# Kernel optimization log

Hardware: AMD Instinct MI355X
Metric: run time of the kernel (lower is better)

Reference implementation:

```python
import jax, jax.numpy as jnp
import numpy as np

EMBED = 512
HEADS = 8
HEAD_DIM = EMBED // HEADS
N, T = 512, 64


def setup_inputs() -> dict:
    key = jax.random.key(0)
    ks = jax.random.split(key, 11)
    s = 1.0 / np.sqrt(EMBED)
    inp = {
        'values': jax.random.normal(ks[0], (N, T, EMBED), jnp.float32),
        'keys':   jax.random.normal(ks[1], (N, T, EMBED), jnp.float32),
        'query':  jax.random.normal(ks[2], (N, T, EMBED), jnp.float32),
        'Wv': jax.random.uniform(ks[3], (EMBED, EMBED), jnp.float32, -s, s),
        'bv': jax.random.uniform(ks[4], (EMBED,), jnp.float32, -s, s),
        'Wk': jax.random.uniform(ks[5], (EMBED, EMBED), jnp.float32, -s, s),
        'bk': jax.random.uniform(ks[6], (EMBED,), jnp.float32, -s, s),
        'Wq': jax.random.uniform(ks[7], (EMBED, EMBED), jnp.float32, -s, s),
        'bq': jax.random.uniform(ks[8], (EMBED,), jnp.float32, -s, s),
        'Wo': jax.random.uniform(ks[9], (EMBED, EMBED), jnp.float32, -s, s),
        'bo': jax.random.uniform(ks[10], (EMBED,), jnp.float32, -s, s),
    }
    return inp


def reference(values, keys, query, Wv, bv, Wk, bk, Wq, bq, Wo, bo):
    n, t, c = query.shape
    v = (values @ Wv.T + bv).reshape(n, t, HEADS, HEAD_DIM)
    k = (keys   @ Wk.T + bk).reshape(n, t, HEADS, HEAD_DIM)
    q = (query  @ Wq.T + bq).reshape(n, t, HEADS, HEAD_DIM)
    # attention over the batch axis: energy[q,k,t,h]
    energy = jnp.einsum('qthd,kthd->qkth', q, k)
    attn = jax.nn.softmax(energy / jnp.sqrt(jnp.float32(EMBED)), axis=1)
    out = jnp.einsum('qkth,kthd->qthd', attn, v).reshape(n, t, HEADS * HEAD_DIM)
    return out @ Wo.T + bo
```

## Files before the change

kernel.cpp:

```cpp
#include <hip/hip_runtime.h>
#include <hip/hip_bf16.h>
#include <math.h>

#define NBATCH 512
#define TT 64
#define EMB 512
#define NHEADS 8
#define HDIM 64
#define MROWS (NBATCH * TT)
#define ROWSTRIDE (TT * EMB)
#define WSEG 262144

static constexpr float QSCALE = 0.0637587140f;

typedef __attribute__((ext_vector_type(8))) short short8v;
typedef __attribute__((ext_vector_type(4))) float f32x4;

__device__ __forceinline__ unsigned short f2bf(float x) {
    union { float f; unsigned int u; } v; v.f = x;
    unsigned int r = v.u + 0x7fff + ((v.u >> 16) & 1);
    return (unsigned short)(r >> 16);
}

__device__ __forceinline__ unsigned int cvtpk(float lo, float hi) {
    unsigned int r;
    asm("v_cvt_pk_bf16_f32 %0, %1, %2" : "=v"(r) : "v"(lo), "v"(hi));
    return r;
}

__device__ __forceinline__ void gl16(const void* g, void* l) {
    __builtin_amdgcn_global_load_lds(
        (const __attribute__((address_space(1))) unsigned int*)g,
        (__attribute__((address_space(3))) unsigned int*)l, 16, 0, 0);
}

__global__ __launch_bounds__(256) void cvtw(
    const float* __restrict__ w0, const float* __restrict__ w1,
    const float* __restrict__ w2, const float* __restrict__ w3,
    unsigned short* __restrict__ dst)
{
    const int seg = blockIdx.y;
    const float* src = (seg == 0) ? w0 : (seg == 1) ? w1 : (seg == 2) ? w2 : w3;
    const float sc = (seg == 0) ? QSCALE : 1.0f;
    const size_t i = (size_t)blockIdx.x * 256 + threadIdx.x;
    float4 v = reinterpret_cast<const float4*>(src)[i];
    ushort4 r;
    r.x = f2bf(v.x * sc); r.y = f2bf(v.y * sc); r.z = f2bf(v.z * sc); r.w = f2bf(v.w * sc);
    reinterpret_cast<ushort4*>(dst + (size_t)seg * WSEG)[i] = r;
}

__global__ __launch_bounds__(256) void gemm_proj3(
    const float* __restrict__ A0, const float* __restrict__ A1,
    const float* __restrict__ A2, const unsigned short* __restrict__ Wb,
    const float* __restrict__ b0, const float* __restrict__ b1, const float* __restrict__ b2,
    unsigned short* __restrict__ o0, unsigned short* __restrict__ o1, unsigned short* __restrict__ o2)
{
    __shared__ __align__(16) float Asf[128 * 32];
    __shared__ __align__(16) unsigned short Bs[128 * 32];
    const int z = blockIdx.z;
    const float* A = (z == 0) ? A0 : (z == 1) ? A1 : A2;
    const unsigned short* W = Wb + (size_t)z * WSEG;
    const float* bias = (z == 0) ? b0 : (z == 1) ? b1 : b2;
    const float bsc = (z == 0) ? QSCALE : 1.0f;
    unsigned short* Cout = (z == 0) ? o0 : (z == 1) ? o1 : o2;

    const int tid = threadIdx.x;
    const int wave = tid >> 6, lane = tid & 63;
    const int lg = lane >> 4, li = lane & 15;
    const int m0 = blockIdx.x * 128;
    const int n0 = blockIdx.y * 128;
    const int wr = (wave >> 1) * 64;
    const int wc = (wave & 1) * 64;

    f32x4 acc[4][4] = {};

    const int asrc_unit = (tid & 7) ^ ((tid >> 3) & 7);
    const float* gaf = A + (size_t)(m0 + (tid >> 3)) * 512 + asrc_unit * 4;
    float* lA = Asf + wave * 256;
    const unsigned short* gb = W + (size_t)(n0 + (tid >> 2)) * 512 + (tid & 3) * 8;
    unsigned short* lB = &Bs[wave * 512];

    for (int k0 = 0; k0 < 512; k0 += 32) {
        __syncthreads();
        gl16(gaf + k0, lA);
        gl16(gaf + k0 + 32 * 512, lA + 1024);
        gl16(gaf + k0 + 64 * 512, lA + 2048);
        gl16(gaf + k0 + 96 * 512, lA + 3072);
        gl16(gb + k0, lB);
        gl16(gb + k0 + 64 * 512, lB + 2048);
        __syncthreads();

        short8v af[4], bfr[4];
#pragma unroll
        for (int i = 0; i < 4; i++) {
            const int r = wr + i * 16 + li;
            const int rx = r & 7;
            const float4 fa = *reinterpret_cast<const float4*>(
                &Asf[r * 32 + ((lg * 2) ^ rx) * 4]);
            const float4 fb = *reinterpret_cast<const float4*>(
                &Asf[r * 32 + ((lg * 2 + 1) ^ rx) * 4]);
            union { unsigned int u[4]; short8v v; } pk;
            pk.u[0] = cvtpk(fa.x, fa.y); pk.u[1] = cvtpk(fa.z, fa.w);
            pk.u[2] = cvtpk(fb.x, fb.y); pk.u[3] = cvtpk(fb.z, fb.w);
            af[i] = pk.v;
            bfr[i] = *reinterpret_cast<const short8v*>(&Bs[(wc + i * 16 + li) * 32 + lg * 8]);
        }
#pragma unroll
        for (int i = 0; i < 4; i++)
#pragma unroll
            for (int j = 0; j < 4; j++)
                acc[i][j] = __builtin_amdgcn_mfma_f32_16x16x32_bf16(af[i], bfr[j], acc[i][j], 0, 0, 0);
    }

#pragma unroll
    for (int j = 0; j < 4; j++) {
        const int col = n0 + wc + j * 16 + li;
        const float bb = bias[col] * bsc;
#pragma unroll
        for (int i = 0; i < 4; i++) {
            const int row0 = m0 + wr + i * 16 + lg * 4;
#pragma unroll
            for (int r = 0; r < 4; r++)
                Cout[(size_t)(row0 + r) * 512 + col] = f2bf(acc[i][j][r] + bb);
        }
    }
}

__global__ __launch_bounds__(256) void gemm_out(
    const unsigned short* __restrict__ A, const unsigned short* __restrict__ W,
    const float* __restrict__ bias, float* __restrict__ Cout)
{
    __shared__ __align__(16) unsigned short As[128 * 32];
    __shared__ __align__(16) unsigned short Bs[128 * 32];
    const int tid = threadIdx.x;
    const int wave = tid >> 6, lane = tid & 63;
    const int lg = lane >> 4, li = lane & 15;
    const int m0 = blockIdx.x * 128;
    const int n0 = blockIdx.y * 128;
    const int wr = (wave >> 1) * 64;
    const int wc = (wave & 1) * 64;

    f32x4 acc[4][4] = {};

    const unsigned short* ga = A + (size_t)(m0 + (tid >> 2)) * 512 + (tid & 3) * 8;
    const unsigned short* gb = W + (size_t)(n0 + (tid >> 2)) * 512 + (tid & 3) * 8;
    unsigned short* lA = &As[wave * 512];
    unsigned short* lB = &Bs[wave * 512];

    for (int k0 = 0; k0 < 512; k0 += 32) {
        __syncthreads();
        gl16(ga + k0, lA);
        gl16(ga + k0 + 64 * 512, lA + 2048);
        gl16(gb + k0, lB);
        gl16(gb + k0 + 64 * 512, lB + 2048);
        __syncthreads();

        short8v af[4], bfr[4];
#pragma unroll
        for (int i = 0; i < 4; i++) {
            af[i]  = *reinterpret_cast<const short8v*>(&As[(wr + i * 16 + li) * 32 + lg * 8]);
            bfr[i] = *reinterpret_cast<const short8v*>(&Bs[(wc + i * 16 + li) * 32 + lg * 8]);
        }
#pragma unroll
        for (int i = 0; i < 4; i++)
#pragma unroll
            for (int j = 0; j < 4; j++)
                acc[i][j] = __builtin_amdgcn_mfma_f32_16x16x32_bf16(af[i], bfr[j], acc[i][j], 0, 0, 0);
    }

#pragma unroll
    for (int j = 0; j < 4; j++) {
        const int col = n0 + wc + j * 16 + li;
        const float bb = bias[col];
#pragma unroll
        for (int i = 0; i < 4; i++) {
            const int row0 = m0 + wr + i * 16 + lg * 4;
#pragma unroll
            for (int r = 0; r < 4; r++)
                Cout[(size_t)(row0 + r) * 512 + col] = acc[i][j][r] + bb;
        }
    }
}

__global__ __launch_bounds__(256) void attn_bf16(
    const unsigned short* __restrict__ qp, const unsigned short* __restrict__ kp,
    const unsigned short* __restrict__ vp, unsigned short* __restrict__ ao)
{
    __shared__ __align__(16) unsigned short Qs[128 * 64];
    __shared__ __align__(16) unsigned short Ks[64 * 64];
    __shared__ __align__(16) unsigned short Vt[64][68];
    __shared__ __align__(16) unsigned short Pl[4][32][72];

    const int tid = threadIdx.x;
    const int wave = tid >> 6, lane = tid & 63;
    const int lg = lane >> 4, li = lane & 15;
    const int n0 = blockIdx.x * 128;
    const int th = blockIdx.y;
    const size_t base = (size_t)(th >> 3) * EMB + (size_t)(th & 7) * HDIM;

    {
        const unsigned short* gq = qp + (size_t)(n0 + (tid >> 3)) * ROWSTRIDE + base + (tid & 7) * 8;
        unsigned short* lq = &Qs[wave * 512];
#pragma unroll
        for (int i = 0; i < 4; i++)
            gl16(gq + (size_t)i * 32 * ROWSTRIDE, lq + i * 2048);
    }
    __syncthreads();
    short8v qf[2][2];
#pragma unroll
    for (int mf = 0; mf < 2; mf++)
#pragma unroll
        for (int kf = 0; kf < 2; kf++)
            qf[mf][kf] = *reinterpret_cast<const short8v*>(
                &Qs[(wave * 32 + mf * 16 + li) * 64 + kf * 32 + lg * 8]);

    const int vd0 = (tid & 15) * 4;
    const int vk0 = (tid >> 4) * 4;
    const unsigned short* gv = vp + base + vd0;
    uint2 vl[4];
#pragma unroll
    for (int i = 0; i < 4; i++)
        vl[i] = *reinterpret_cast<const uint2*>(gv + (size_t)(vk0 + i) * ROWSTRIDE);

    const short8v ones = (short8v)(short)0x3F80;
    f32x4 acc[2][4] = {};
    f32x4 acc_l[2] = {};

    for (int kv = 0; kv < 8; kv++) {
        const int k0 = kv * 64;
        __syncthreads();

        {
            unsigned short* lk = &Ks[wave * 512];
#pragma unroll
            for (int i = 0; i < 2; i++) {
                const int r = (tid >> 3) + i * 32;
                const int srcofs = (((tid & 7) * 8) ^ ((r & 7) * 8));
                gl16(kp + (size_t)(k0 + r) * ROWSTRIDE + base + srcofs, lk + i * 2048);
            }
        }
#pragma unroll
        for (int dd = 0; dd < 4; dd++) {
            const unsigned int sel = (dd & 1) ? 0x07060302u : 0x05040100u;
            const unsigned int a = (dd < 2) ? vl[0].x : vl[0].y;
            const unsigned int b = (dd < 2) ? vl[1].x : vl[1].y;
            const unsigned int c = (dd < 2) ? vl[2].x : vl[2].y;
            const unsigned int d = (dd < 2) ? vl[3].x : vl[3].y;
            uint2 o;
            o.x = __builtin_amdgcn_perm(b, a, sel);
            o.y = __builtin_amdgcn_perm(d, c, sel);
            *reinterpret_cast<uint2*>(&Vt[vd0 + dd][vk0]) = o;
        }
        __syncthreads();

        if (kv < 7) {
#pragma unroll
            for (int i = 0; i < 4; i++)
                vl[i] = *reinterpret_cast<const uint2*>(
                    gv + (size_t)(k0 + 64 + vk0 + i) * ROWSTRIDE);
        }

        f32x4 s[2][4] = {};
#pragma unroll
        for (int nf = 0; nf < 4; nf++) {
            const int key = nf * 16 + li;
#pragma unroll
            for (int kf = 0; kf < 2; kf++) {
                const short8v kfrag = *reinterpret_cast<const short8v*>(
                    &Ks[key * 64 + ((kf * 32 + lg * 8) ^ ((key & 7) * 8))]);
#pragma unroll
                for (int mf = 0; mf < 2; mf++)
                    s[mf][nf] = __builtin_amdgcn_mfma_f32_16x16x32_bf16(kfrag, qf[mf][kf], s[mf][nf], 0, 0, 0);
            }
        }

#pragma unroll
        for (int mf = 0; mf < 2; mf++)
#pragma unroll
            for (int nf = 0; nf < 4; nf++) {
                const float p0 = exp2f(s[mf][nf][0]);
                const float p1 = exp2f(s[mf][nf][1]);
                const float p2 = exp2f(s[mf][nf][2]);
                const float p3 = exp2f(s[mf][nf][3]);
                union { unsigned int u[2]; uint2 v; } pk2;
                pk2.u[0] = cvtpk(p0, p1);
                pk2.u[1] = cvtpk(p2, p3);
                *reinterpret_cast<uint2*>(&Pl[wave][mf * 16 + li][nf * 16 + lg * 4]) = pk2.v;
            }

        short8v pf[2][2];
#pragma unroll
        for (int mf = 0; mf < 2; mf++)
#pragma unroll
            for (int kf = 0; kf < 2; kf++)
                pf[mf][kf] = *reinterpret_cast<const short8v*>(
                    &Pl[wave][mf * 16 + li][kf * 32 + lg * 8]);
#pragma unroll
        for (int mf = 0; mf < 2; mf++)
#pragma unroll
            for (int kf = 0; kf < 2; kf++)
                acc_l[mf] = __builtin_amdgcn_mfma_f32_16x16x32_bf16(pf[mf][kf], ones, acc_l[mf], 0, 0, 0);

#pragma unroll
        for (int df = 0; df < 4; df++)
#pragma unroll
            for (int kf = 0; kf < 2; kf++) {
                const short8v vfr = *reinterpret_cast<const short8v*>(
                    &Vt[df * 16 + li][kf * 32 + lg * 8]);
#pragma unroll
                for (int mf = 0; mf < 2; mf++)
                    acc[mf][df] = __builtin_amdgcn_mfma_f32_16x16x32_bf16(pf[mf][kf], vfr, acc[mf][df], 0, 0, 0);
            }
    }

#pragma unroll
    for (int mf = 0; mf < 2; mf++) {
#pragma unroll
        for (int r = 0; r < 4; r++) {
            const float linv = 1.0f / acc_l[mf][r];
            const int qrow = n0 + wave * 32 + mf * 16 + lg * 4 + r;
#pragma unroll
            for (int df = 0; df < 4; df++)
                ao[(size_t)qrow * ROWSTRIDE + base + df * 16 + li] = f2bf(acc[mf][df][r] * linv);
        }
    }
}

extern "C" void kernel_launch(void* const* d_in, const int* in_sizes, int n_in,
                              void* d_out, int out_size, void* d_ws, size_t ws_size,
                              hipStream_t stream) {
    const float* values = (const float*)d_in[0];
    const float* keys   = (const float*)d_in[1];
    const float* query  = (const float*)d_in[2];
    const float* Wv = (const float*)d_in[3];
    const float* bv = (const float*)d_in[4];
    const float* Wk = (const float*)d_in[5];
    const float* bk = (const float*)d_in[6];
    const float* Wq = (const float*)d_in[7];
    const float* bq = (const float*)d_in[8];
    const float* Wo = (const float*)d_in[9];
    const float* bo = (const float*)d_in[10];
    float* out = (float*)d_out;

    unsigned short* ws16 = (unsigned short*)d_ws;
    const size_t PLANE = (size_t)MROWS * EMB;
    unsigned short* qb = ws16;
    unsigned short* kb = ws16 + PLANE;
    unsigned short* vb = ws16 + 2 * PLANE;
    unsigned short* ab = ws16 + 3 * PLANE;
    unsigned short* wb = ws16 + 4 * PLANE;

    cvtw<<<dim3(WSEG / 4 / 256, 4), 256, 0, stream>>>(Wq, Wk, Wv, Wo, wb);

    gemm_proj3<<<dim3(MROWS / 128, EMB / 128, 3), 256, 0, stream>>>(
        query, keys, values, wb, bq, bk, bv, qb, kb, vb);

    attn_bf16<<<dim3(4, TT * NHEADS), 256, 0, stream>>>(qb, kb, vb, ab);

    gemm_out<<<dim3(MROWS / 128, EMB / 128), 256, 0, stream>>>(
        ab, wb + 3 * WSEG, bo, out);
}
```

Measured before the change: 245.0 us.

## Widen projection GEMM tile to full output width with 512-thread blocks

```diff
diff --git a/kernel.cpp b/kernel.cpp
--- a/kernel.cpp
+++ b/kernel.cpp
@@ -49,15 +49,15 @@
     reinterpret_cast<ushort4*>(dst + (size_t)seg * WSEG)[i] = r;
 }
 
-__global__ __launch_bounds__(256) void gemm_proj3(
+__global__ __launch_bounds__(512) void gemm_proj3(
     const float* __restrict__ A0, const float* __restrict__ A1,
     const float* __restrict__ A2, const unsigned short* __restrict__ Wb,
     const float* __restrict__ b0, const float* __restrict__ b1, const float* __restrict__ b2,
     unsigned short* __restrict__ o0, unsigned short* __restrict__ o1, unsigned short* __restrict__ o2)
 {
-    __shared__ __align__(16) float Asf[128 * 32];
-    __shared__ __align__(16) unsigned short Bs[128 * 32];
-    const int z = blockIdx.z;
+    __shared__ __align__(16) float Asf[128 * 64];
+    __shared__ __align__(16) unsigned short Bs[512 * 64];
+    const int z = blockIdx.y;
     const float* A = (z == 0) ? A0 : (z == 1) ? A1 : A2;
     const unsigned short* W = Wb + (size_t)z * WSEG;
     const float* bias = (z == 0) ? b0 : (z == 1) ? b1 : b2;
@@ -68,57 +68,61 @@
     const int wave = tid >> 6, lane = tid & 63;
     const int lg = lane >> 4, li = lane & 15;
     const int m0 = blockIdx.x * 128;
-    const int n0 = blockIdx.y * 128;
-    const int wr = (wave >> 1) * 64;
-    const int wc = (wave & 1) * 64;
-
-    f32x4 acc[4][4] = {};
-
-    const int asrc_unit = (tid & 7) ^ ((tid >> 3) & 7);
-    const float* gaf = A + (size_t)(m0 + (tid >> 3)) * 512 + asrc_unit * 4;
+    const int wm = (wave >> 2) * 64;
+    const int wn = (wave & 3) * 128;
+
+    f32x4 acc[4][8] = {};
+
+    const int au = (tid & 15) ^ ((tid >> 4) & 15);
+    const float* gaf = A + (size_t)(m0 + (tid >> 4)) * 512 + au * 4;
     float* lA = Asf + wave * 256;
-    const unsigned short* gb = W + (size_t)(n0 + (tid >> 2)) * 512 + (tid & 3) * 8;
-    unsigned short* lB = &Bs[wave * 512];
-
-    for (int k0 = 0; k0 < 512; k0 += 32) {
-        __syncthreads();
-        gl16(gaf + k0, lA);
-        gl16(gaf + k0 + 32 * 512, lA + 1024);
-        gl16(gaf + k0 + 64 * 512, lA + 2048);
-        gl16(gaf + k0 + 96 * 512, lA + 3072);
-        gl16(gb + k0, lB);
-        gl16(gb + k0 + 64 * 512, lB + 2048);
-        __syncthreads();
-
-        short8v af[4], bfr[4];
+    const unsigned short* gb = W + (size_t)(tid >> 3) * 512 + (tid & 7) * 8;
+    unsigned short* lB = Bs + wave * 512;
+
+    for (int k0 = 0; k0 < 512; k0 += 64) {
+        __syncthreads();
+#pragma unroll
+        for (int i = 0; i < 4; i++)
+            gl16(gaf + k0 + (size_t)i * 32 * 512, lA + i * 2048);
+#pragma unroll
+        for (int i = 0; i < 8; i++)
+            gl16(gb + k0 + (size_t)i * 64 * 512, lB + i * 4096);
+        __syncthreads();
+
+#pragma unroll
+        for (int kk = 0; kk < 2; kk++) {
+            short8v af[4];
+#pragma unroll
+            for (int i = 0; i < 4; i++) {
+                const int r = wm + i * 16 + li;
+                const int lu0 = kk * 8 + lg * 2;
+                const float4 fa = *reinterpret_cast<const float4*>(
+                    &Asf[r * 64 + (lu0 ^ li) * 4]);
+                const float4 fb = *reinterpret_cast<const float4*>(
+                    &Asf[r * 64 + ((lu0 + 1) ^ li) * 4]);
+                union { unsigned int u[4]; short8v v; } pk;
+                pk.u[0] = cvtpk(fa.x, fa.y); pk.u[1] = cvtpk(fa.z, fa.w);
+                pk.u[2] = cvtpk(fb.x, fb.y); pk.u[3] = cvtpk(fb.z, fb.w);
+                af[i] = pk.v;
+            }
+#pragma unroll
+            for (int j = 0; j < 8; j++) {
+                const short8v bfr = *reinterpret_cast<const short8v*>(
+                    &Bs[(wn + j * 16 + li) * 64 + kk * 32 + lg * 8]);
+#pragma unroll
+                for (int i = 0; i < 4; i++)
+                    acc[i][j] = __builtin_amdgcn_mfma_f32_16x16x32_bf16(af[i], bfr, acc[i][j], 0, 0, 0);
+            }
+        }
+    }
+
+#pragma unroll
+    for (int j = 0; j < 8; j++) {
+        const int col = wn + j * 16 + li;
+        const float bb = bias[col] * bsc;
 #pragma unroll
         for (int i = 0; i < 4; i++) {
-            const int r = wr + i * 16 + li;
-            const int rx = r & 7;
-            const float4 fa = *reinterpret_cast<const float4*>(
-                &Asf[r * 32 + ((lg * 2) ^ rx) * 4]);
-            const float4 fb = *reinterpret_cast<const float4*>(
-                &Asf[r * 32 + ((lg * 2 + 1) ^ rx) * 4]);
-            union { unsigned int u[4]; short8v v; } pk;
-            pk.u[0] = cvtpk(fa.x, fa.y); pk.u[1] = cvtpk(fa.z, fa.w);
-            pk.u[2] = cvtpk(fb.x, fb.y); pk.u[3] = cvtpk(fb.z, fb.w);
-            af[i] = pk.v;
-            bfr[i] = *reinterpret_cast<const short8v*>(&Bs[(wc + i * 16 + li) * 32 + lg * 8]);
-        }
-#pragma unroll
-        for (int i = 0; i < 4; i++)
-#pragma unroll
-            for (int j = 0; j < 4; j++)
-                acc[i][j] = __builtin_amdgcn_mfma_f32_16x16x32_bf16(af[i], bfr[j], acc[i][j], 0, 0, 0);
-    }
-
-#pragma unroll
-    for (int j = 0; j < 4; j++) {
-        const int col = n0 + wc + j * 16 + li;
-        const float bb = bias[col] * bsc;
-#pragma unroll
-        for (int i = 0; i < 4; i++) {
-            const int row0 = m0 + wr + i * 16 + lg * 4;
+            const int row0 = m0 + wm + i * 16 + lg * 4;
 #pragma unroll
             for (int r = 0; r < 4; r++)
                 Cout[(size_t)(row0 + r) * 512 + col] = f2bf(acc[i][j][r] + bb);
@@ -352,7 +356,7 @@
 
     cvtw<<<dim3(WSEG / 4 / 256, 4), 256, 0, stream>>>(Wq, Wk, Wv, Wo, wb);
 
-    gemm_proj3<<<dim3(MROWS / 128, EMB / 128, 3), 256, 0, stream>>>(
+    gemm_proj3<<<dim3(MROWS / 128, 3), 512, 0, stream>>>(
         query, keys, values, wb, bq, bk, bv, qb, kb, vb);
 
     attn_bf16<<<dim3(4, TT * NHEADS), 256, 0, stream>>>(qb, kb, vb, ab);
```

New measurement: 223.8 us. 8.6% less time.

## Retile QKV projection GEMM to full-width 64-row blocks with single fp32 A read

Applied to the files above, without the earlier changes.

```diff
diff --git a/kernel.cpp b/kernel.cpp
--- a/kernel.cpp
+++ b/kernel.cpp
@@ -49,15 +49,15 @@
     reinterpret_cast<ushort4*>(dst + (size_t)seg * WSEG)[i] = r;
 }
 
-__global__ __launch_bounds__(256) void gemm_proj3(
+__global__ __launch_bounds__(512) void gemm_proj3(
     const float* __restrict__ A0, const float* __restrict__ A1,
     const float* __restrict__ A2, const unsigned short* __restrict__ Wb,
     const float* __restrict__ b0, const float* __restrict__ b1, const float* __restrict__ b2,
     unsigned short* __restrict__ o0, unsigned short* __restrict__ o1, unsigned short* __restrict__ o2)
 {
-    __shared__ __align__(16) float Asf[128 * 32];
-    __shared__ __align__(16) unsigned short Bs[128 * 32];
-    const int z = blockIdx.z;
+    __shared__ __align__(16) unsigned short Ws[512 * 32];
+    __shared__ __align__(16) unsigned short Ab[64 * 40];
+    const int z = blockIdx.y;
     const float* A = (z == 0) ? A0 : (z == 1) ? A1 : A2;
     const unsigned short* W = Wb + (size_t)z * WSEG;
     const float* bias = (z == 0) ? b0 : (z == 1) ? b1 : b2;
@@ -67,58 +67,52 @@
     const int tid = threadIdx.x;
     const int wave = tid >> 6, lane = tid & 63;
     const int lg = lane >> 4, li = lane & 15;
-    const int m0 = blockIdx.x * 128;
-    const int n0 = blockIdx.y * 128;
-    const int wr = (wave >> 1) * 64;
-    const int wc = (wave & 1) * 64;
+    const int m0 = blockIdx.x * 64;
 
     f32x4 acc[4][4] = {};
 
-    const int asrc_unit = (tid & 7) ^ ((tid >> 3) & 7);
-    const float* gaf = A + (size_t)(m0 + (tid >> 3)) * 512 + asrc_unit * 4;
-    float* lA = Asf + wave * 256;
-    const unsigned short* gb = W + (size_t)(n0 + (tid >> 2)) * 512 + (tid & 3) * 8;
-    unsigned short* lB = &Bs[wave * 512];
+    const unsigned short* gw = W
+        + (size_t)((wave << 4) + (lane >> 2)) * 512 + (lane & 3) * 8;
+    unsigned short* lW = Ws + wave * 512;
+    const float* ga = A + (size_t)(m0 + (tid >> 3)) * 512 + (tid & 7) * 4;
+    const int ar = tid >> 3;
+    const int au = tid & 7;
 
     for (int k0 = 0; k0 < 512; k0 += 32) {
         __syncthreads();
-        gl16(gaf + k0, lA);
-        gl16(gaf + k0 + 32 * 512, lA + 1024);
-        gl16(gaf + k0 + 64 * 512, lA + 2048);
-        gl16(gaf + k0 + 96 * 512, lA + 3072);
-        gl16(gb + k0, lB);
-        gl16(gb + k0 + 64 * 512, lB + 2048);
-        __syncthreads();
-
-        short8v af[4], bfr[4];
+#pragma unroll
+        for (int i = 0; i < 4; i++)
+            gl16(gw + k0 + (size_t)i * 128 * 512, lW + i * 4096);
+        {
+            const float4 f = *reinterpret_cast<const float4*>(ga + k0);
+            union { unsigned int u[2]; uint2 v; } pk;
+            pk.u[0] = cvtpk(f.x, f.y);
+            pk.u[1] = cvtpk(f.z, f.w);
+            *reinterpret_cast<uint2*>(&Ab[ar * 40 + au * 4]) = pk.v;
+        }
+        __syncthreads();
+
+        short8v af[4], wf[4];
 #pragma unroll
         for (int i = 0; i < 4; i++) {
-            const int r = wr + i * 16 + li;
-            const int rx = r & 7;
-            const float4 fa = *reinterpret_cast<const float4*>(
-                &Asf[r * 32 + ((lg * 2) ^ rx) * 4]);
-            const float4 fb = *reinterpret_cast<const float4*>(
-                &Asf[r * 32 + ((lg * 2 + 1) ^ rx) * 4]);
-            union { unsigned int u[4]; short8v v; } pk;
-            pk.u[0] = cvtpk(fa.x, fa.y); pk.u[1] = cvtpk(fa.z, fa.w);
-            pk.u[2] = cvtpk(fb.x, fb.y); pk.u[3] = cvtpk(fb.z, fb.w);
-            af[i] = pk.v;
-            bfr[i] = *reinterpret_cast<const short8v*>(&Bs[(wc + i * 16 + li) * 32 + lg * 8]);
+            af[i] = *reinterpret_cast<const short8v*>(&Ab[(i * 16 + li) * 40 + lg * 8]);
+            wf[i] = *reinterpret_cast<const short8v*>(
+                &Ws[(wave * 64 + i * 16 + li) * 32 + lg * 8]);
         }
 #pragma unroll
         for (int i = 0; i < 4; i++)
 #pragma unroll
             for (int j = 0; j < 4; j++)
-                acc[i][j] = __builtin_amdgcn_mfma_f32_16x16x32_bf16(af[i], bfr[j], acc[i][j], 0, 0, 0);
+                acc[i][j] = __builtin_amdgcn_mfma_f32_16x16x32_bf16(af[i], wf[j], acc[i][j], 0, 0, 0);
     }
 
 #pragma unroll
     for (int j = 0; j < 4; j++) {
-        const int col = n0 + wc + j * 16 + li;
+        const int col = wave * 64 + j * 16 + li;
         const float bb = bias[col] * bsc;
 #pragma unroll
         for (int i = 0; i < 4; i++) {
-            const int row0 = m0 + wr + i * 16 + lg * 4;
+            const int row0 = m0 + i * 16 + lg * 4;
 #pragma unroll
             for (int r = 0; r < 4; r++)
                 Cout[(size_t)(row0 + r) * 512 + col] = f2bf(acc[i][j][r] + bb);
@@ -352,7 +346,7 @@
 
     cvtw<<<dim3(WSEG / 4 / 256, 4), 256, 0, stream>>>(Wq, Wk, Wv, Wo, wb);
 
-    gemm_proj3<<<dim3(MROWS / 128, EMB / 128, 3), 256, 0, stream>>>(
+    gemm_proj3<<<dim3(MROWS / 64, 3), 512, 0, stream>>>(
         query, keys, values, wb, bq, bk, bv, qb, kb, vb);
 
     attn_bf16<<<dim3(4, TT * NHEADS), 256, 0, stream>>>(qb, kb, vb, ab);
```

Result: slower. 262.5 us (+7.2%).
